# Optimization experiments

Hardware: AMD Instinct MI355X
Metric: run time of the kernel (lower is better)

The kernel has to match this reference:

```python
import jax, jax.numpy as jnp
import numpy as np

B, S, HID = 2, 2048, 2048
H, KH, D = 16, 4, 128  # heads, kv heads, head_dim
N_REP = H // KH
SCALE = D ** -0.5


def rotate_half(x):
    x1, x2 = x[..., : D // 2], x[..., D // 2:]
    return jnp.concatenate((-x2, x1), axis=-1)


def setup_inputs() -> dict:
    key = jax.random.key(0)
    ks = jax.random.split(key, 6)
    hidden_states = jax.random.normal(ks[0], (B, S, HID), jnp.float32)
    # standard RoPE cos/sin tables, shape [B, S, D]
    inv_freq = 1.0 / (10000.0 ** (np.arange(0, D, 2, dtype=np.float32) / D))
    pos = np.arange(S, dtype=np.float32)
    freqs = np.outer(pos, inv_freq)            # [S, D/2]
    emb = np.concatenate([freqs, freqs], -1)   # [S, D]
    cos = jnp.broadcast_to(jnp.cos(emb), (B, S, D)).astype(jnp.float32)
    sin = jnp.broadcast_to(jnp.sin(emb), (B, S, D)).astype(jnp.float32)
    # additive causal mask [1, 1, S, S]
    neg = jnp.finfo(jnp.float32).min
    causal = jnp.triu(jnp.full((S, S), neg, jnp.float32), k=1)
    attention_mask = causal[None, None]
    std = 0.02
    wq = jax.random.normal(ks[1], (HID, H * D), jnp.float32) * std
    wk = jax.random.normal(ks[2], (HID, KH * D), jnp.float32) * std
    wv = jax.random.normal(ks[3], (HID, KH * D), jnp.float32) * std
    wo = jax.random.normal(ks[4], (H * D, HID), jnp.float32) * std
    return {"hidden_states": hidden_states, "cos": cos, "sin": sin,
            "attention_mask": attention_mask, "wq": wq, "wk": wk, "wv": wv, "wo": wo}


def reference(hidden_states, cos, sin, attention_mask, wq, wk, wv, wo):
    b, s, _ = hidden_states.shape
    q = (hidden_states @ wq).reshape(b, s, H, D).transpose(0, 2, 1, 3)   # [b,H,s,d]
    k = (hidden_states @ wk).reshape(b, s, KH, D).transpose(0, 2, 1, 3)  # [b,KH,s,d]
    v = (hidden_states @ wv).reshape(b, s, KH, D).transpose(0, 2, 1, 3)
    c = cos[:, None, :, :]  # [b,1,s,d] broadcast over heads
    sn = sin[:, None, :, :]
    q = q * c + rotate_half(q) * sn
    k = k * c + rotate_half(k) * sn
    # GQA: repeat KV heads
    k = jnp.repeat(k, N_REP, axis=1)  # [b,H,s,d]
    v = jnp.repeat(v, N_REP, axis=1)
    scores = jnp.einsum('bhqd,bhkd->bhqk', q, k) * SCALE + attention_mask
    probs = jax.nn.softmax(scores, axis=-1)
    attn = jnp.einsum('bhqk,bhkd->bhqd', probs, v)
    attn = attn.transpose(0, 2, 1, 3).reshape(b, s, H * D)
    return attn @ wo
```

## Files before the change

kernel.cpp:

```cpp
#include <hip/hip_runtime.h>
#include <stdint.h>

#define Bc   2
#define Sc   2048
#define HIDc 2048
#define Hc   16
#define KHc  4
#define Dc   128
#define HDc  2048
#define KHDc 512
#define QKVS 3072
#define SCALE2c 0.12751744657f
#define M0c 6.0f
#define N_ITEMS 1536

typedef _Float16 f16;
typedef _Float16 f16x2 __attribute__((ext_vector_type(2)));
typedef _Float16 f16x4 __attribute__((ext_vector_type(4)));
typedef _Float16 f16x8 __attribute__((ext_vector_type(8)));
typedef float    f32x4 __attribute__((ext_vector_type(4)));

__device__ __forceinline__ void gl_lds16(const void* g, void* l) {
  __builtin_amdgcn_global_load_lds(
      (const __attribute__((address_space(1))) unsigned int*)g,
      (__attribute__((address_space(3))) unsigned int*)l, 16, 0, 0);
}

__global__ __launch_bounds__(256) void conv_hs(const float* __restrict__ in,
                                               f16* __restrict__ out,
                                               int* __restrict__ ctr) {
  if (blockIdx.x == 0 && threadIdx.x == 0) *ctr = 0;
  int i = (blockIdx.x * 256 + threadIdx.x) * 4;
  float4 v = *(const float4*)&in[i];
  f16x4 o; o[0] = (f16)v.x; o[1] = (f16)v.y; o[2] = (f16)v.z; o[3] = (f16)v.w;
  *(f16x4*)&out[i] = o;
}

__global__ __launch_bounds__(256) void trw_all(const float* __restrict__ wq,
                                               const float* __restrict__ wk,
                                               const float* __restrict__ wv,
                                               const float* __restrict__ wo,
                                               f16* __restrict__ wqkvT,
                                               f16* __restrict__ woT) {
  const int z = blockIdx.z;
  const float* in; f16* out; int C, rowOff;
  if (z == 0)      { in = wq; out = wqkvT; C = 2048; rowOff = 0; }
  else if (z == 1) { in = wk; out = wqkvT; C = 512;  rowOff = 2048; }
  else if (z == 2) { in = wv; out = wqkvT; C = 512;  rowOff = 2560; }
  else             { in = wo; out = woT;   C = 2048; rowOff = 0; }
  if (blockIdx.x * 64 >= C) return;
  __shared__ float Ld[64 * 65];
  const int tid = threadIdx.x;
  const int r0 = blockIdx.y * 64, c0 = blockIdx.x * 64;
#pragma unroll
  for (int p = 0; p < 4; ++p) {
    int idx = p * 256 + tid;
    int r = idx >> 4, c4 = (idx & 15) * 4;
    float4 v = *(const float4*)&in[(size_t)(r0 + r) * C + c0 + c4];
    Ld[r * 65 + c4 + 0] = v.x; Ld[r * 65 + c4 + 1] = v.y;
    Ld[r * 65 + c4 + 2] = v.z; Ld[r * 65 + c4 + 3] = v.w;
  }
  __syncthreads();
#pragma unroll
  for (int p = 0; p < 4; ++p) {
    int idx = p * 256 + tid;
    int oc = idx >> 4, m4 = (idx & 15) * 4;
    f16x4 o;
#pragma unroll
    for (int i = 0; i < 4; ++i) o[i] = (f16)Ld[(m4 + i) * 65 + oc];
    *(f16x4*)&out[(size_t)(rowOff + c0 + oc) * 2048 + r0 + m4] = o;
  }
}

__global__ __launch_bounds__(256) void rope_all(f16* __restrict__ x,
                                                const float* __restrict__ cb,
                                                const float* __restrict__ sb) {
  int bid = blockIdx.x;
  int colbase, log2h, idx;
  if (bid < 16384) { colbase = 0;    log2h = 4; idx = bid * 256 + threadIdx.x; }
  else             { colbase = 2048; log2h = 2; idx = (bid - 16384) * 256 + threadIdx.x; }
  int d   = idx & 63;
  int h   = (idx >> 6) & ((1 << log2h) - 1);
  int row = idx >> (6 + log2h);
  f16* p = x + (size_t)row * QKVS + colbase + h * 128;
  float x1 = (float)p[d], x2 = (float)p[64 + d];
  float c = cb[(size_t)row * 128 + d], s = sb[(size_t)row * 128 + d];
  p[d]      = (f16)(x1 * c - x2 * s);
  p[64 + d] = (f16)(x2 * c + x1 * s);
}

__global__ __launch_bounds__(256) void v_tr(const f16* __restrict__ QKV,
                                            f16* __restrict__ Vt) {
  __shared__ f16 Ld[64 * 78];
  const int tid = threadIdx.x;
  const int s0 = blockIdx.x * 64, d0 = blockIdx.y * 64;
  const int b = blockIdx.z >> 2, kh = blockIdx.z & 3;
#pragma unroll
  for (int p = 0; p < 2; ++p) {
    int idx = p * 256 + tid;
    int sl = idx >> 3, dc8 = (idx & 7) * 8;
    f16x8 v = *(const f16x8*)&QKV[(size_t)(b * Sc + s0 + sl) * QKVS + 2560 + kh * 128 + d0 + dc8];
#pragma unroll
    for (int i = 0; i < 4; ++i) {
      f16x2 w; w[0] = v[2 * i]; w[1] = v[2 * i + 1];
      *(f16x2*)&Ld[sl * 78 + dc8 + 2 * i] = w;
    }
  }
  __syncthreads();
  {
    int dr = (tid >> 3) * 2, sc8 = (tid & 7) * 8;
    f16x8 r0v, r1v;
#pragma unroll
    for (int j = 0; j < 8; ++j) {
      f16x2 w = *(const f16x2*)&Ld[(sc8 + j) * 78 + dr];
      r0v[j] = w[0]; r1v[j] = w[1];
    }
    size_t obase = ((size_t)(b * KHc + kh) * 128 + d0 + dr) * Sc + s0 + sc8;
    *(f16x8*)&Vt[obase]      = r0v;
    *(f16x8*)&Vt[obase + Sc] = r1v;
  }
}

template<int NREP, int CF16>
__global__ __launch_bounds__(512, 2) void gemm8p(const f16* __restrict__ A,
                                                 const f16* __restrict__ Bt,
                                                 void* __restrict__ Cout,
                                                 int K, int cstride) {
  __shared__ f16 Al[2][16384];
  __shared__ f16 Bl[2][NREP * 4096];
  const int tid  = threadIdx.x;
  const int lane = tid & 63, wave = tid >> 6;
  const int quad = lane >> 4, l16 = lane & 15;
  const int wm = wave >> 2, wn = wave & 3;
  const int m0 = blockIdx.y * 256, n0 = blockIdx.x * (NREP * 64);
  f32x4 acc[8][NREP] = {};

  auto stage = [&](int buf, int k0) {
#pragma unroll
    for (int p = 0; p < 4; ++p) {
      const int g  = wave * 2 + (p >> 1);
      const int kq = (p & 1) * 4 + quad;
      gl_lds16(&A[(size_t)(m0 + g * 16 + l16) * K + k0 + kq * 8],
               &Al[buf][(wave * 4 + p) * 512]);
    }
#pragma unroll
    for (int p = 0; p < NREP; ++p) {
      const int gb = wave * NREP + p;
      const int gi = gb >> 1, kh2 = gb & 1;
      gl_lds16(&Bt[(size_t)(n0 + gi * 16 + l16) * K + k0 + kh2 * 32 + quad * 8],
               &Bl[buf][gb * 512]);
    }
  };

  stage(0, 0);
  const int NT = K >> 6;
  for (int t = 0; t < NT; ++t) {
    const int cur = t & 1;
    __syncthreads();
    if (t + 1 < NT) stage(cur ^ 1, (t + 1) * 64);

    f16x8 bf[NREP][2];
#pragma unroll
    for (int j = 0; j < NREP; ++j)
#pragma unroll
      for (int ks = 0; ks < 2; ++ks)
        bf[j][ks] = *(const f16x8*)&Bl[cur][(((wn * NREP + j) * 8 + ks * 4 + quad) * 16 + l16) * 8];
#pragma unroll
    for (int mh = 0; mh < 2; ++mh) {
      f16x8 af[4][2];
#pragma unroll
      for (int i = 0; i < 4; ++i)
#pragma unroll
        for (int ks = 0; ks < 2; ++ks)
          af[i][ks] = *(const f16x8*)&Al[cur][(((wm * 8 + mh * 4 + i) * 8 + ks * 4 + quad) * 16 + l16) * 8];
      __builtin_amdgcn_s_setprio(1);
#pragma unroll
      for (int ks = 0; ks < 2; ++ks)
#pragma unroll
        for (int i = 0; i < 4; ++i)
#pragma unroll
          for (int j = 0; j < NREP; ++j)
            acc[mh * 4 + i][j] = __builtin_amdgcn_mfma_f32_16x16x32_f16(
                af[i][ks], bf[j][ks], acc[mh * 4 + i][j], 0, 0, 0);
      __builtin_amdgcn_s_setprio(0);
    }
  }

  const int rbase = m0 + wm * 128;
  const int cbase = n0 + wn * NREP * 16;
#pragma unroll
  for (int mi = 0; mi < 8; ++mi)
#pragma unroll
    for (int j = 0; j < NREP; ++j)
#pragma unroll
      for (int r = 0; r < 4; ++r) {
        size_t idx = (size_t)(rbase + mi * 16 + quad * 4 + r) * cstride + cbase + j * 16 + l16;
        if (CF16) ((f16*)Cout)[idx]   = (f16)acc[mi][j][r];
        else      ((float*)Cout)[idx] = acc[mi][j][r];
      }
}

__global__ __launch_bounds__(256, 4) void attn_v6(const f16* __restrict__ QKV,
                                                  const f16* __restrict__ Vt,
                                                  f16* __restrict__ Ob,
                                                  f16* __restrict__ Opart,
                                                  float2* __restrict__ ML,
                                                  int* __restrict__ ctr) {
  __shared__ f16 Kl[64 * 128];
  __shared__ f16 Vl[64 * 128];
  __shared__ f16 Ps[4 * 512];
  __shared__ int item_s;
  const int tid  = threadIdx.x;
  const int lane = tid & 63, wave = tid >> 6;
  const int quad = lane >> 4, l16 = lane & 15;

  f16x8 ones_f;
#pragma unroll
  for (int i = 0; i < 8; ++i) ones_f[i] = (l16 == 0) ? (f16)1.0f : (f16)0.0f;

  for (;;) {
    if (tid == 0) item_s = atomicAdd(ctr, 1);
    __syncthreads();
    const int item = item_s;
    if (item >= N_ITEMS) break;

    int qt, bh, k0t, k1t, hf = -1;
    if (item < 1280) {
      int base = 0, c = 32;
#pragma unroll 1
      for (; c >= 17; --c) {
        int sz = (c & 1) ? 64 : 96;
        if (item < base + sz) break;
        base += sz;
      }
      int off = item - base;
      if (off < 64) {
        qt = c - 1; hf = off >> 5; bh = off & 31;
        int nk = qt + 1, hn = nk >> 1;
        k0t = hf ? hn : 0; k1t = hf ? nk : hn;
      } else {
        qt = (c >> 1) - 1; bh = off - 64; k0t = 0; k1t = qt + 1;
      }
    } else {
      int off = item - 1280;
      qt = 7 - (off >> 5); bh = off & 31; k0t = 0; k1t = qt + 1;
    }
    const int b = bh >> 4, h = bh & 15, kh = h >> 2;
    const int qbase = qt * 64 + wave * 16;

    f16x8 qf[4];
    {
      const f16* qp = QKV + (size_t)(b * Sc + qbase + l16) * QKVS + h * 128 + quad * 8;
#pragma unroll
      for (int c = 0; c < 4; ++c) qf[c] = *(const f16x8*)(qp + c * 32);
    }
    f32x4 ls = {};
    f32x4 o[8] = {};

    auto stageK = [&](int kt) {
#pragma unroll
      for (int p = 0; p < 4; ++p)
        gl_lds16(&QKV[(size_t)(b * Sc + kt * 64 + wave * 16 + l16) * QKVS + 2048 + kh * 128 + p * 32 + quad * 8],
                 &Kl[(wave * 4 + p) * 512]);
    };
    auto stageV = [&](int kt) {
#pragma unroll
      for (int p = 0; p < 4; ++p) {
        const int dt = wave * 2 + (p >> 1), kc = p & 1;
        gl_lds16(&Vt[(size_t)((b * KHc + kh) * 128 + dt * 16 + l16) * Sc + kt * 64 + kc * 32 + quad * 8],
                 &Vl[(wave * 4 + p) * 512]);
      }
    };

    stageK(k0t);
    stageV(k0t);

    for (int kt = k0t; kt < k1t; ++kt) {
      const bool more = (kt + 1 < k1t);

      asm volatile("s_waitcnt vmcnt(4)" ::: "memory");
      __builtin_amdgcn_sched_barrier(0);
      __builtin_amdgcn_s_barrier();
      __builtin_amdgcn_sched_barrier(0);

      __builtin_amdgcn_s_setprio(1);
      f32x4 s4[4] = {};
#pragma unroll
      for (int kc = 0; kc < 2; ++kc)
#pragma unroll
        for (int c = 0; c < 4; ++c) {
          f16x8 ka = *(const f16x8*)&Kl[(((kc * 2 + 0) * 4 + c) * 4 + quad) * 128 + l16 * 8];
          f16x8 kb = *(const f16x8*)&Kl[(((kc * 2 + 1) * 4 + c) * 4 + quad) * 128 + l16 * 8];
          s4[kc * 2 + 0] = __builtin_amdgcn_mfma_f32_16x16x32_f16(qf[c], ka, s4[kc * 2 + 0], 0, 0, 0);
          s4[kc * 2 + 1] = __builtin_amdgcn_mfma_f32_16x16x32_f16(qf[c], kb, s4[kc * 2 + 1], 0, 0, 0);
        }
      __builtin_amdgcn_s_setprio(0);

      __builtin_amdgcn_sched_barrier(0);
      __builtin_amdgcn_s_barrier();
      __builtin_amdgcn_sched_barrier(0);
      if (more) stageK(kt + 1);

      const bool diag = (kt == qt);
      const int cb = kt * 64 + l16;
      const int wb  = wave * 512 + (l16 & 7);
      const int rhi = l16 >> 3;
      float e2[4], e3[4];
#pragma unroll
      for (int r = 0; r < 4; ++r) {
        float v0 = fmaf(s4[0][r], SCALE2c, -M0c);
        float v1 = fmaf(s4[1][r], SCALE2c, -M0c);
        float v2 = fmaf(s4[2][r], SCALE2c, -M0c);
        float v3 = fmaf(s4[3][r], SCALE2c, -M0c);
        if (diag) {
          const int qrow = qbase + quad * 4 + r;
          if (cb      > qrow) v0 = -1e30f;
          if (cb + 16 > qrow) v1 = -1e30f;
          if (cb + 32 > qrow) v2 = -1e30f;
          if (cb + 48 > qrow) v3 = -1e30f;
        }
        float p0 = exp2f(v0), p1 = exp2f(v1);
        e2[r] = exp2f(v2); e3[r] = exp2f(v3);
        const int rowoff = (quad * 4 + r) * 8;
        Ps[wb + (rhi + 0) * 128 + rowoff] = (f16)p0;
        Ps[wb + (rhi + 2) * 128 + rowoff] = (f16)p1;
      }

      if (more) { asm volatile("s_waitcnt vmcnt(4)" ::: "memory"); }
      else      { asm volatile("s_waitcnt vmcnt(0)" ::: "memory"); }
      __builtin_amdgcn_sched_barrier(0);
      __builtin_amdgcn_s_barrier();
      __builtin_amdgcn_sched_barrier(0);

      {
        f16x8 pf = *(const f16x8*)&Ps[wave * 512 + quad * 128 + l16 * 8];
        __builtin_amdgcn_s_setprio(1);
        ls = __builtin_amdgcn_mfma_f32_16x16x32_f16(pf, ones_f, ls, 0, 0, 0);
#pragma unroll
        for (int dt = 0; dt < 8; ++dt) {
          f16x8 vf = *(const f16x8*)&Vl[((dt * 2 + 0) * 4 + quad) * 128 + l16 * 8];
          o[dt] = __builtin_amdgcn_mfma_f32_16x16x32_f16(pf, vf, o[dt], 0, 0, 0);
        }
        __builtin_amdgcn_s_setprio(0);
      }
#pragma unroll
      for (int r = 0; r < 4; ++r) {
        const int rowoff = (quad * 4 + r) * 8;
        Ps[wb + (rhi + 0) * 128 + rowoff] = (f16)e2[r];
        Ps[wb + (rhi + 2) * 128 + rowoff] = (f16)e3[r];
      }
      {
        f16x8 pf = *(const f16x8*)&Ps[wave * 512 + quad * 128 + l16 * 8];
        __builtin_amdgcn_s_setprio(1);
        ls = __builtin_amdgcn_mfma_f32_16x16x32_f16(pf, ones_f, ls, 0, 0, 0);
#pragma unroll
        for (int dt = 0; dt < 8; ++dt) {
          f16x8 vf = *(const f16x8*)&Vl[((dt * 2 + 1) * 4 + quad) * 128 + l16 * 8];
          o[dt] = __builtin_amdgcn_mfma_f32_16x16x32_f16(pf, vf, o[dt], 0, 0, 0);
        }
        __builtin_amdgcn_s_setprio(0);
      }

      __builtin_amdgcn_sched_barrier(0);
      __builtin_amdgcn_s_barrier();
      __builtin_amdgcn_sched_barrier(0);
      if (more) stageV(kt + 1);
    }

    float inv[4], lrow[4];
#pragma unroll
    for (int r = 0; r < 4; ++r) {
      lrow[r] = __shfl(ls[r], lane & 48);
      inv[r] = 1.0f / lrow[r];
    }
    if (hf < 0) {
#pragma unroll
      for (int dt = 0; dt < 8; ++dt)
#pragma unroll
        for (int r = 0; r < 4; ++r)
          Ob[(size_t)(b * Sc + qbase + quad * 4 + r) * HDc + h * 128 + dt * 16 + l16] =
              (f16)(o[dt][r] * inv[r]);
    } else {
      const int tile = (qt - 16) * 32 + bh;
      f16* op = Opart + ((size_t)tile * 2 + hf) * (64 * 128);
#pragma unroll
      for (int dt = 0; dt < 8; ++dt)
#pragma unroll
        for (int r = 0; r < 4; ++r)
          op[(wave * 16 + quad * 4 + r) * 128 + dt * 16 + l16] = (f16)(o[dt][r] * inv[r]);
      if (l16 == 0) {
#pragma unroll
        for (int r = 0; r < 4; ++r) {
          float2 ml; ml.x = M0c; ml.y = lrow[r];
          ML[((size_t)tile * 2 + hf) * 64 + wave * 16 + quad * 4 + r] = ml;
        }
      }
    }
  }
}

__global__ __launch_bounds__(256) void attn_merge(const f16* __restrict__ Opart,
                                                  const float2* __restrict__ ML,
                                                  f16* __restrict__ Ob) {
  const int tile = blockIdx.x;
  const int qt = 16 + (tile >> 5), bh = tile & 31;
  const int b = bh >> 4, h = bh & 15;
  const int tid = threadIdx.x;
  const int row = tid >> 2, c0 = (tid & 3) * 32;
  float2 ml1 = ML[(size_t)tile * 2 * 64 + row];
  float2 ml2 = ML[((size_t)tile * 2 + 1) * 64 + row];
  float m = fmaxf(ml1.x, ml2.x);
  float w1 = ml1.y * exp2f(ml1.x - m);
  float w2 = ml2.y * exp2f(ml2.x - m);
  float rinv = 1.0f / (w1 + w2);
  float a1 = w1 * rinv, a2 = w2 * rinv;
  const f16* o1 = Opart + (size_t)tile * 2 * (64 * 128) + row * 128 + c0;
  const f16* o2 = o1 + 64 * 128;
  f16* out = Ob + (size_t)(b * Sc + qt * 64 + row) * HDc + h * 128 + c0;
#pragma unroll
  for (int j = 0; j < 4; ++j) {
    f16x8 x1 = *(const f16x8*)(o1 + j * 8);
    f16x8 x2 = *(const f16x8*)(o2 + j * 8);
    f16x8 y;
#pragma unroll
    for (int i = 0; i < 8; ++i) y[i] = (f16)(a1 * (float)x1[i] + a2 * (float)x2[i]);
    *(f16x8*)(out + j * 8) = y;
  }
}

extern "C" void kernel_launch(void* const* d_in, const int* in_sizes, int n_in,
                              void* d_out, int out_size, void* d_ws, size_t ws_size,
                              hipStream_t stream) {
  (void)in_sizes; (void)n_in; (void)out_size; (void)ws_size;
  const float* hs   = (const float*)d_in[0];
  const float* cosb = (const float*)d_in[1];
  const float* sinb = (const float*)d_in[2];
  const float* wq = (const float*)d_in[4];
  const float* wk = (const float*)d_in[5];
  const float* wv = (const float*)d_in[6];
  const float* wo = (const float*)d_in[7];
  float* out = (float*)d_out;

  char* ws = (char*)d_ws;
  int*  ctr = (int*)ws;
  size_t off = 256;
  auto alloc = [&](size_t bytes) { char* p = ws + off; off += (bytes + 255) & ~(size_t)255; return p; };
  f16*  hsF   = (f16*)alloc((size_t)Bc * Sc * HIDc * 2);
  f16*  woT   = (f16*)alloc((size_t)HIDc * HDc * 2);
  f16*  QKVf  = (f16*)alloc((size_t)Bc * Sc * QKVS * 2);
  f16*  Vt_g  = (f16*)alloc((size_t)Bc * KHc * Dc * Sc * 2);
  f16*  wqkvT = (f16*)alloc((size_t)QKVS * HIDc * 2);
  f16*  Opart = wqkvT;
  {
    size_t opart_bytes = (size_t)512 * 2 * 64 * 128 * 2;
    size_t wqkvT_bytes = (size_t)QKVS * HIDc * 2;
    if (opart_bytes > wqkvT_bytes) off += opart_bytes - wqkvT_bytes;
  }
  float2* ML = (float2*)alloc((size_t)512 * 2 * 64 * sizeof(float2));
  f16*  attnF = hsF;

  conv_hs<<<8192, 256, 0, stream>>>(hs, hsF, ctr);
  trw_all<<<dim3(32, 32, 4), 256, 0, stream>>>(wq, wk, wv, wo, wqkvT, woT);

  gemm8p<3, 1><<<dim3(16, 16), 512, 0, stream>>>(hsF, wqkvT, QKVf, 2048, QKVS);

  rope_all<<<20480, 256, 0, stream>>>(QKVf, cosb, sinb);
  v_tr<<<dim3(32, 2, 8), 256, 0, stream>>>(QKVf, Vt_g);

  attn_v6<<<1024, 256, 0, stream>>>(QKVf, Vt_g, attnF, Opart, ML, ctr);
  attn_merge<<<512, 256, 0, stream>>>(Opart, ML, attnF);

  gemm8p<2, 0><<<dim3(16, 16), 512, 0, stream>>>(attnF, woT, out, 2048, 2048);
}
```

Baseline: 411.3 us.

## Pair query tiles per 512-thread block sharing double-buffered K/V staging

The attention kernel now launches 512-thread blocks in which two groups of four waves handle adjacent query tiles. Both groups share one K/V tile staged into double-buffered LDS, which halves global K/V traffic per query tile and replaces the split K/V staging with a single prefetch of the next tile. The work-item schedule is rebuilt around tile pairs. In exchange, the lower query tile idles on the last key tile of each pair, the larger LDS footprint limits how many blocks fit per CU, and the hand-placed vmcnt waits give way to plain __syncthreads.

```diff
diff --git a/kernel.cpp b/kernel.cpp
--- a/kernel.cpp
+++ b/kernel.cpp
@@ -12,7 +12,7 @@
 #define QKVS 3072
 #define SCALE2c 0.12751744657f
 #define M0c 6.0f
-#define N_ITEMS 1536
+#define N_ITEMS2 768
 
 typedef _Float16 f16;
 typedef _Float16 f16x2 __attribute__((ext_vector_type(2)));
@@ -200,19 +200,20 @@
       }
 }
 
-__global__ __launch_bounds__(256, 4) void attn_v6(const f16* __restrict__ QKV,
+__global__ __launch_bounds__(512, 4) void attn_v7(const f16* __restrict__ QKV,
                                                   const f16* __restrict__ Vt,
                                                   f16* __restrict__ Ob,
                                                   f16* __restrict__ Opart,
                                                   float2* __restrict__ ML,
                                                   int* __restrict__ ctr) {
-  __shared__ f16 Kl[64 * 128];
-  __shared__ f16 Vl[64 * 128];
-  __shared__ f16 Ps[4 * 512];
+  __shared__ f16 Kl[2][8192];
+  __shared__ f16 Vl[2][8192];
+  __shared__ f16 Ps[8 * 512];
   __shared__ int item_s;
   const int tid  = threadIdx.x;
   const int lane = tid & 63, wave = tid >> 6;
   const int quad = lane >> 4, l16 = lane & 15;
+  const int qsel = wave >> 2, wv = wave & 3;
 
   f16x8 ones_f;
 #pragma unroll
@@ -222,31 +223,32 @@
     if (tid == 0) item_s = atomicAdd(ctr, 1);
     __syncthreads();
     const int item = item_s;
-    if (item >= N_ITEMS) break;
-
-    int qt, bh, k0t, k1t, hf = -1;
-    if (item < 1280) {
-      int base = 0, c = 32;
+    if (item >= N_ITEMS2) break;
+
+    int p, bh, k0t, k1t, hf = -1;
+    if (item < 640) {
+      int base = 0, c = 16;
 #pragma unroll 1
-      for (; c >= 17; --c) {
+      for (; c >= 9; --c) {
         int sz = (c & 1) ? 64 : 96;
         if (item < base + sz) break;
         base += sz;
       }
       int off = item - base;
       if (off < 64) {
-        qt = c - 1; hf = off >> 5; bh = off & 31;
-        int nk = qt + 1, hn = nk >> 1;
-        k0t = hf ? hn : 0; k1t = hf ? nk : hn;
+        p = c - 1; hf = off >> 5; bh = off & 31;
+        int hn = p + 1;
+        k0t = hf ? hn : 0; k1t = hf ? 2 * p + 2 : hn;
       } else {
-        qt = (c >> 1) - 1; bh = off - 64; k0t = 0; k1t = qt + 1;
+        p = (c >> 1) - 1; bh = off - 64; k0t = 0; k1t = 2 * p + 2;
       }
     } else {
-      int off = item - 1280;
-      qt = 7 - (off >> 5); bh = off & 31; k0t = 0; k1t = qt + 1;
+      int off = item - 640;
+      p = 3 - (off >> 5); bh = off & 31; k0t = 0; k1t = 2 * p + 2;
     }
     const int b = bh >> 4, h = bh & 15, kh = h >> 2;
-    const int qbase = qt * 64 + wave * 16;
+    const int qt = 2 * p + qsel;
+    const int qbase = qt * 64 + wv * 16;
 
     f16x8 qf[4];
     {
@@ -257,31 +259,28 @@
     f32x4 ls = {};
     f32x4 o[8] = {};
 
-    auto stageK = [&](int kt) {
-#pragma unroll
-      for (int p = 0; p < 4; ++p)
-        gl_lds16(&QKV[(size_t)(b * Sc + kt * 64 + wave * 16 + l16) * QKVS + 2048 + kh * 128 + p * 32 + quad * 8],
-                 &Kl[(wave * 4 + p) * 512]);
+    auto stageKV = [&](int kt, int buf) {
+#pragma unroll
+      for (int p2 = 0; p2 < 2; ++p2) {
+        const int g = wave * 2 + p2;
+        gl_lds16(&QKV[(size_t)(b * Sc + kt * 64 + (g >> 2) * 16 + l16) * QKVS + 2048 + kh * 128 + (g & 3) * 32 + quad * 8],
+                 &Kl[buf][g * 512]);
+      }
+#pragma unroll
+      for (int p2 = 0; p2 < 2; ++p2) {
+        const int g = wave * 2 + p2;
+        gl_lds16(&Vt[(size_t)((b * KHc + kh) * 128 + (g >> 1) * 16 + l16) * Sc + kt * 64 + (g & 1) * 32 + quad * 8],
+                 &Vl[buf][g * 512]);
+      }
     };
-    auto stageV = [&](int kt) {
-#pragma unroll
-      for (int p = 0; p < 4; ++p) {
-        const int dt = wave * 2 + (p >> 1), kc = p & 1;
-        gl_lds16(&Vt[(size_t)((b * KHc + kh) * 128 + dt * 16 + l16) * Sc + kt * 64 + kc * 32 + quad * 8],
-                 &Vl[(wave * 4 + p) * 512]);
-      }
-    };
-
-    stageK(k0t);
-    stageV(k0t);
+
+    stageKV(k0t, 0);
 
     for (int kt = k0t; kt < k1t; ++kt) {
-      const bool more = (kt + 1 < k1t);
-
-      asm volatile("s_waitcnt vmcnt(4)" ::: "memory");
-      __builtin_amdgcn_sched_barrier(0);
-      __builtin_amdgcn_s_barrier();
-      __builtin_amdgcn_sched_barrier(0);
+      const int cur = (kt - k0t) & 1;
+      __syncthreads();
+      if (kt + 1 < k1t) stageKV(kt + 1, cur ^ 1);
+      if (kt > qt) continue;
 
       __builtin_amdgcn_s_setprio(1);
       f32x4 s4[4] = {};
@@ -289,17 +288,12 @@
       for (int kc = 0; kc < 2; ++kc)
 #pragma unroll
         for (int c = 0; c < 4; ++c) {
-          f16x8 ka = *(const f16x8*)&Kl[(((kc * 2 + 0) * 4 + c) * 4 + quad) * 128 + l16 * 8];
-          f16x8 kb = *(const f16x8*)&Kl[(((kc * 2 + 1) * 4 + c) * 4 + quad) * 128 + l16 * 8];
+          f16x8 ka = *(const f16x8*)&Kl[cur][(((kc * 2 + 0) * 4 + c) * 4 + quad) * 128 + l16 * 8];
+          f16x8 kb = *(const f16x8*)&Kl[cur][(((kc * 2 + 1) * 4 + c) * 4 + quad) * 128 + l16 * 8];
           s4[kc * 2 + 0] = __builtin_amdgcn_mfma_f32_16x16x32_f16(qf[c], ka, s4[kc * 2 + 0], 0, 0, 0);
           s4[kc * 2 + 1] = __builtin_amdgcn_mfma_f32_16x16x32_f16(qf[c], kb, s4[kc * 2 + 1], 0, 0, 0);
         }
       __builtin_amdgcn_s_setprio(0);
-
-      __builtin_amdgcn_sched_barrier(0);
-      __builtin_amdgcn_s_barrier();
-      __builtin_amdgcn_sched_barrier(0);
-      if (more) stageK(kt + 1);
 
       const bool diag = (kt == qt);
       const int cb = kt * 64 + l16;
@@ -326,19 +320,13 @@
         Ps[wb + (rhi + 2) * 128 + rowoff] = (f16)p1;
       }
 
-      if (more) { asm volatile("s_waitcnt vmcnt(4)" ::: "memory"); }
-      else      { asm volatile("s_waitcnt vmcnt(0)" ::: "memory"); }
-      __builtin_amdgcn_sched_barrier(0);
-      __builtin_amdgcn_s_barrier();
-      __builtin_amdgcn_sched_barrier(0);
-
       {
         f16x8 pf = *(const f16x8*)&Ps[wave * 512 + quad * 128 + l16 * 8];
         __builtin_amdgcn_s_setprio(1);
         ls = __builtin_amdgcn_mfma_f32_16x16x32_f16(pf, ones_f, ls, 0, 0, 0);
 #pragma unroll
         for (int dt = 0; dt < 8; ++dt) {
-          f16x8 vf = *(const f16x8*)&Vl[((dt * 2 + 0) * 4 + quad) * 128 + l16 * 8];
+          f16x8 vf = *(const f16x8*)&Vl[cur][((dt * 2 + 0) * 4 + quad) * 128 + l16 * 8];
           o[dt] = __builtin_amdgcn_mfma_f32_16x16x32_f16(pf, vf, o[dt], 0, 0, 0);
         }
         __builtin_amdgcn_s_setprio(0);
@@ -355,16 +343,11 @@
         ls = __builtin_amdgcn_mfma_f32_16x16x32_f16(pf, ones_f, ls, 0, 0, 0);
 #pragma unroll
         for (int dt = 0; dt < 8; ++dt) {
-          f16x8 vf = *(const f16x8*)&Vl[((dt * 2 + 1) * 4 + quad) * 128 + l16 * 8];
+          f16x8 vf = *(const f16x8*)&Vl[cur][((dt * 2 + 1) * 4 + quad) * 128 + l16 * 8];
           o[dt] = __builtin_amdgcn_mfma_f32_16x16x32_f16(pf, vf, o[dt], 0, 0, 0);
         }
         __builtin_amdgcn_s_setprio(0);
       }
-
-      __builtin_amdgcn_sched_barrier(0);
-      __builtin_amdgcn_s_barrier();
-      __builtin_amdgcn_sched_barrier(0);
-      if (more) stageV(kt + 1);
     }
 
     float inv[4], lrow[4];
@@ -373,6 +356,7 @@
       lrow[r] = __shfl(ls[r], lane & 48);
       inv[r] = 1.0f / lrow[r];
     }
+    const int rl = wv * 16 + quad * 4;
     if (hf < 0) {
 #pragma unroll
       for (int dt = 0; dt < 8; ++dt)
@@ -387,12 +371,12 @@
       for (int dt = 0; dt < 8; ++dt)
 #pragma unroll
         for (int r = 0; r < 4; ++r)
-          op[(wave * 16 + quad * 4 + r) * 128 + dt * 16 + l16] = (f16)(o[dt][r] * inv[r]);
+          op[(rl + r) * 128 + dt * 16 + l16] = (f16)(o[dt][r] * inv[r]);
       if (l16 == 0) {
 #pragma unroll
         for (int r = 0; r < 4; ++r) {
           float2 ml; ml.x = M0c; ml.y = lrow[r];
-          ML[((size_t)tile * 2 + hf) * 64 + wave * 16 + quad * 4 + r] = ml;
+          ML[((size_t)tile * 2 + hf) * 64 + rl + r] = ml;
         }
       }
     }
@@ -467,7 +451,7 @@
   rope_all<<<20480, 256, 0, stream>>>(QKVf, cosb, sinb);
   v_tr<<<dim3(32, 2, 8), 256, 0, stream>>>(QKVf, Vt_g);
 
-  attn_v6<<<1024, 256, 0, stream>>>(QKVf, Vt_g, attnF, Opart, ML, ctr);
+  attn_v7<<<512, 512, 0, stream>>>(QKVf, Vt_g, attnF, Opart, ML, ctr);
   attn_merge<<<512, 256, 0, stream>>>(Opart, ML, attnF);
 
   gemm8p<2, 0><<<dim3(16, 16), 512, 0, stream>>>(attnF, woT, out, 2048, 2048);
```

New measurement: 395.0 us. 1.04x faster.
